# Performance work log

Hardware: AMD Instinct MI355X
Metric: run time of the kernel (lower is better)

The kernel has to match this reference:

```python
import jax, jax.numpy as jnp
import numpy as np

NUM_HEADS = 16
HIDDEN = 1024
HEAD_DIM = HIDDEN // NUM_HEADS


def setup_inputs() -> dict:
    key = jax.random.key(0)
    ks = jax.random.split(key, 8)
    B, S = 4, 1024
    scale = 0.02
    return {
        "hidden_states": jax.random.normal(ks[0], (B, S, HIDDEN), jnp.float32),
        "attention_mask": jnp.zeros((B, 1, 1, S), jnp.float32),
        "Wq": jax.random.normal(ks[1], (HIDDEN, HIDDEN), jnp.float32) * scale,
        "bq": jnp.zeros((HIDDEN,), jnp.float32),
        "Wk": jax.random.normal(ks[2], (HIDDEN, HIDDEN), jnp.float32) * scale,
        "bk": jnp.zeros((HIDDEN,), jnp.float32),
        "Wv": jax.random.normal(ks[3], (HIDDEN, HIDDEN), jnp.float32) * scale,
        "bv": jnp.zeros((HIDDEN,), jnp.float32),
    }


def _split_heads(x):
    # [B,S,H] -> [B,heads,S,head_dim]
    B, S, _ = x.shape
    return x.reshape(B, S, NUM_HEADS, HEAD_DIM).transpose(0, 2, 1, 3)


def reference(hidden_states, attention_mask, Wq, bq, Wk, bk, Wv, bv):
    # torch.nn.Linear convention: y = x @ W.T + b
    q = _split_heads(hidden_states @ Wq.T + bq)
    k = _split_heads(hidden_states @ Wk.T + bk)
    v = _split_heads(hidden_states @ Wv.T + bv)
    scores = jnp.einsum('bhqd,bhkd->bhqk', q, k) * (HEAD_DIM ** -0.5)
    scores = scores + attention_mask  # broadcast [B,1,1,S]
    probs = jax.nn.softmax(scores, axis=-1)
    context = jnp.einsum('bhqk,bhkd->bhqd', probs, v)  # [B,heads,S,head_dim]
    B, _, S, _ = context.shape
    return context.transpose(0, 2, 1, 3).reshape(B, S, HIDDEN)
```

## Files before the change

kernel.cpp:

```cpp
#include <hip/hip_runtime.h>
#include <hip/hip_bf16.h>
#include <stdint.h>

#define NH 16
#define HID 1024
#define HD 64
#define NB 4
#define SS 1024
#define MTOT (NB*SS)

typedef __attribute__((ext_vector_type(8))) short bf16x8;
typedef __attribute__((ext_vector_type(4))) float f32x4;
typedef __attribute__((ext_vector_type(16))) float f32x16;

#define LOG2E 1.44269504088896f

__device__ __forceinline__ unsigned short f2bf(float f) {
  union { float f; unsigned u; } v; v.f = f;
  unsigned u = v.u;
  return (unsigned short)((u + 0x7FFFu + ((u >> 16) & 1u)) >> 16);
}

__device__ __forceinline__ unsigned cvtpk(float lo, float hi) {
  unsigned r;
  asm("v_cvt_pk_bf16_f32 %0, %1, %2" : "=v"(r) : "v"(lo), "v"(hi));
  return r;
}

__device__ __forceinline__ void pl32swap(unsigned &a, unsigned &b) {
  asm("v_permlane32_swap_b32 %0, %1" : "+v"(a), "+v"(b));
}

__device__ __forceinline__ float exp2fast(float x) {
  float r;
  asm("v_exp_f32 %0, %1" : "=v"(r) : "v"(x));
  return r;
}

__device__ __forceinline__ void async16(void* lds, const void* g) {
  __builtin_amdgcn_global_load_lds(
      (const __attribute__((address_space(1))) unsigned*)g,
      (__attribute__((address_space(3))) unsigned*)lds, 16, 0, 0);
}

__global__ void cvt_all(const float4* __restrict__ X,
                        const float4* __restrict__ Wq,
                        const float4* __restrict__ Wk,
                        const float4* __restrict__ Wv,
                        ushort4* __restrict__ Xb,
                        ushort4* __restrict__ Wb) {
  int i = blockIdx.x * 256 + threadIdx.x;
  const float4* src; ushort4* dst; int idx;
  if (i < (MTOT * HID / 4)) {
    src = X; dst = Xb; idx = i;
  } else {
    int j = i - (MTOT * HID / 4);
    int sel = j >> 18;
    idx = j & 262143;
    src = (sel == 0) ? Wq : (sel == 1) ? Wk : Wv;
    dst = Wb + (size_t)sel * 262144;
  }
  float4 v = src[idx];
  ushort4 o;
  o.x = f2bf(v.x); o.y = f2bf(v.y); o.z = f2bf(v.z); o.w = f2bf(v.w);
  dst[idx] = o;
}

__global__ __launch_bounds__(256) void qkv_gemm(
    const ushort* __restrict__ Xb,
    const ushort* __restrict__ Wb,
    const float* __restrict__ bq,
    const float* __restrict__ bk,
    const float* __restrict__ bv,
    ushort* __restrict__ Q,
    ushort* __restrict__ K,
    ushort* __restrict__ Vt)
{
  __shared__ __attribute__((aligned(16))) ushort Al[2][128 * 32];
  __shared__ __attribute__((aligned(16))) ushort Bl[2][128 * 32];

  int bid = blockIdx.x;
  int swz = (bid & 7) * 96 + (bid >> 3);
  const int nbn = 3072 / 128;
  int bm = swz / nbn, bn = swz % nbn;
  int m0 = bm * 128, n0 = bn * 128;

  int tid = threadIdx.x;
  int wave = tid >> 6, lane = tid & 63;
  int g = lane >> 4, c = lane & 15;
  int wr = wave >> 1, wc = wave & 1;

  int srow = tid >> 2;
  int schunk = tid & 3;
  int ssw = (srow >> 1) & 3;
  const ushort* Asrc0 = Xb + (size_t)(m0 + srow) * 1024 + ((schunk ^ ssw) << 3);
  const ushort* Asrc1 = Xb + (size_t)(m0 + 64 + srow) * 1024 + ((schunk ^ ssw) << 3);
  const ushort* Bsrc0 = Wb + (size_t)(n0 + srow) * 1024 + ((schunk ^ ssw) << 3);
  const ushort* Bsrc1 = Wb + (size_t)(n0 + 64 + srow) * 1024 + ((schunk ^ ssw) << 3);
  int soff = srow * 64 + schunk * 16;

#define GSTAGE(bi) do {                                   \
    char* la_ = (char*)Al[bi]; char* lb_ = (char*)Bl[bi]; \
    async16(la_ + soff,        Asrc0);                    \
    async16(la_ + 4096 + soff, Asrc1);                    \
    async16(lb_ + soff,        Bsrc0);                    \
    async16(lb_ + 4096 + soff, Bsrc1);                    \
    Asrc0 += 32; Asrc1 += 32; Bsrc0 += 32; Bsrc1 += 32;   \
  } while (0)

  f32x4 acc[4][4] = {};
  int rsw = (c >> 1) & 3;
  int ch = ((g ^ rsw) << 4);

  GSTAGE(0);

  for (int ks = 0; ks < 32; ++ks) {
    int cur = ks & 1;
    if (ks < 31) {
      GSTAGE(cur ^ 1);
      asm volatile("s_waitcnt vmcnt(4)" ::: "memory");
    } else {
      asm volatile("s_waitcnt vmcnt(0)" ::: "memory");
    }
    __builtin_amdgcn_sched_barrier(0);
    __builtin_amdgcn_s_barrier();
    __builtin_amdgcn_sched_barrier(0);

    const char* la = (const char*)Al[cur];
    const char* lb = (const char*)Bl[cur];
    bf16x8 a[4], b[4];
    #pragma unroll
    for (int m = 0; m < 4; ++m)
      a[m] = *(const bf16x8*)(la + (wr * 64 + m * 16 + c) * 64 + ch);
    #pragma unroll
    for (int n = 0; n < 4; ++n)
      b[n] = *(const bf16x8*)(lb + (wc * 64 + n * 16 + c) * 64 + ch);
    __builtin_amdgcn_s_setprio(1);
    #pragma unroll
    for (int m = 0; m < 4; ++m)
      #pragma unroll
      for (int n = 0; n < 4; ++n)
        acc[m][n] = __builtin_amdgcn_mfma_f32_16x16x32_bf16(a[m], b[n], acc[m][n], 0, 0, 0);
    __builtin_amdgcn_s_setprio(0);

    __builtin_amdgcn_sched_barrier(0);
    __builtin_amdgcn_s_barrier();
  }
#undef GSTAGE

  int sel = n0 >> 10;
  const float* bp = (sel == 0) ? bq : (sel == 1) ? bk : bv;
  float scl = (sel == 0) ? 0.125f * LOG2E : 1.0f;

  #pragma unroll
  for (int n = 0; n < 4; ++n) {
    int nn = (n0 & 1023) + wc * 64 + n * 16 + c;
    float bias = bp[nn];
    int h = nn >> 6, d = nn & 63;
    #pragma unroll
    for (int m = 0; m < 4; ++m) {
      int rowg = m0 + wr * 64 + m * 16 + g * 4;
      int bb = rowg >> 10;
      int s = rowg & 1023;
      #pragma unroll
      for (int r = 0; r < 4; ++r) {
        float val = (acc[m][n][r] + bias) * scl;
        unsigned short ob = f2bf(val);
        if (sel == 0)
          Q[(size_t)((bb * 16 + h) * 1024 + s + r) * 64 + d] = ob;
        else if (sel == 1)
          K[(size_t)((bb * 16 + h) * 1024 + s + r) * 64 + d] = ob;
        else
          Vt[(size_t)((bb * 16 + h) * 64 + d) * 1024 + s + r] = ob;
      }
    }
  }
}

__device__ __forceinline__ void build_pa(const f32x16& p, bf16x8& pa0, bf16x8& pa1) {
  unsigned W0 = cvtpk(p[0],  p[1]);
  unsigned W1 = cvtpk(p[2],  p[3]);
  unsigned W2 = cvtpk(p[4],  p[5]);
  unsigned W3 = cvtpk(p[6],  p[7]);
  unsigned W4 = cvtpk(p[8],  p[9]);
  unsigned W5 = cvtpk(p[10], p[11]);
  unsigned W6 = cvtpk(p[12], p[13]);
  unsigned W7 = cvtpk(p[14], p[15]);
  pl32swap(W0, W2);
  pl32swap(W1, W3);
  pl32swap(W4, W6);
  pl32swap(W5, W7);
  union { unsigned u[4]; bf16x8 v; } a0, a1;
  a0.u[0] = W0; a0.u[1] = W1; a0.u[2] = W2; a0.u[3] = W3;
  a1.u[0] = W4; a1.u[1] = W5; a1.u[2] = W6; a1.u[3] = W7;
  pa0 = a0.v; pa1 = a1.v;
}

__global__ __launch_bounds__(256) void attn(
    const ushort* __restrict__ Q,
    const ushort* __restrict__ K,
    const ushort* __restrict__ Vt,
    const float* __restrict__ mask,
    float* __restrict__ out)
{
  __shared__ __attribute__((aligned(16))) char kv_lds[2][16384];

  int blk = blockIdx.x;
  int xcd = blk & 7;
  int j = blk >> 3;
  int bh = xcd * 8 + (j >> 3);
  int qt = j & 7;
  int b = bh >> 4, h = bh & 15;
  int tid = threadIdx.x, wave = tid >> 6, lane = tid & 63;
  int r31 = lane & 31, hi = lane >> 5;
  int rsw = r31 & 7;
  int hib = hi << 4;
  int q0 = qt * 128 + wave * 32;

  const ushort* Qb = Q + (size_t)bh * SS * 64;
  const ushort* Kb = K + (size_t)bh * SS * 64;
  const ushort* Vb = Vt + (size_t)bh * 64 * SS;
  const float* mb = mask + b * SS;

  bf16x8 qf[4];
  #pragma unroll
  for (int kp = 0; kp < 4; ++kp)
    qf[kp] = *(const bf16x8*)(Qb + (size_t)(q0 + r31) * 64 + kp * 16 + hi * 8);

  int srow = lane >> 3;
  int schunk = lane & 7;
  const ushort* sptr[4];
  int soff[4];
  #pragma unroll
  for (int j2 = 0; j2 < 4; ++j2) {
    soff[j2] = wave * 4096 + j2 * 1024;
    if (wave < 2) {
      int row = wave * 32 + j2 * 8 + srow;
      sptr[j2] = Kb + (size_t)row * 64 + ((schunk ^ srow) << 3);
    } else {
      int d = (wave - 2) * 32 + j2 * 8 + srow;
      sptr[j2] = Vb + (size_t)d * SS + ((schunk ^ srow) << 3);
    }
  }
  const int sstep = (wave < 2) ? 64 * 64 : 64;

#define STAGE(bufidx) do {                              \
    char* lb_ = kv_lds[bufidx];                         \
    async16(lb_ + soff[0], sptr[0]);                    \
    async16(lb_ + soff[1], sptr[1]);                    \
    async16(lb_ + soff[2], sptr[2]);                    \
    async16(lb_ + soff[3], sptr[3]);                    \
    sptr[0] += sstep; sptr[1] += sstep;                 \
    sptr[2] += sstep; sptr[3] += sstep;                 \
  } while (0)

  f32x16 o0 = (f32x16)0.0f, o1 = (f32x16)0.0f;
  float mrow = 0.f, lrow = 0.f;

  STAGE(0);

  for (int it = 0; it < 16; ++it) {
    int cur = it & 1;
    if (it < 15) {
      STAGE(cur ^ 1);
      asm volatile("s_waitcnt vmcnt(4)" ::: "memory");
    } else {
      asm volatile("s_waitcnt vmcnt(0)" ::: "memory");
    }
    __builtin_amdgcn_sched_barrier(0);
    __builtin_amdgcn_s_barrier();
    __builtin_amdgcn_sched_barrier(0);

    const char* kb0 = kv_lds[cur];
    const char* vb0 = kv_lds[cur] + 8192;

    f32x16 s0 = (f32x16)0.0f, s1 = (f32x16)0.0f;
    __builtin_amdgcn_s_setprio(1);
    #pragma unroll
    for (int kp = 0; kp < 4; ++kp) {
      int ch = (((kp << 1) | hi) ^ rsw) << 4;
      bf16x8 ka = *(const bf16x8*)(kb0 + r31 * 128 + ch);
      bf16x8 kc = *(const bf16x8*)(kb0 + (32 + r31) * 128 + ch);
      s0 = __builtin_amdgcn_mfma_f32_32x32x16_bf16(ka, qf[kp], s0, 0, 0, 0);
      s1 = __builtin_amdgcn_mfma_f32_32x32x16_bf16(kc, qf[kp], s1, 0, 0, 0);
    }
    __builtin_amdgcn_s_setprio(0);

    int kv = it * 64;
    #pragma unroll
    for (int sq = 0; sq < 4; ++sq) {
      f32x4 mk0 = *(const f32x4*)(mb + kv + sq * 8 + hi * 4);
      f32x4 mk1 = *(const f32x4*)(mb + kv + 32 + sq * 8 + hi * 4);
      #pragma unroll
      for (int r = 0; r < 4; ++r) {
        s0[sq * 4 + r] = fmaf(mk0[r], LOG2E, s0[sq * 4 + r]);
        s1[sq * 4 + r] = fmaf(mk1[r], LOG2E, s1[sq * 4 + r]);
      }
    }

    float mx = s0[0];
    #pragma unroll
    for (int i = 1; i < 16; ++i) mx = fmaxf(mx, s0[i]);
    #pragma unroll
    for (int i = 0; i < 16; ++i) mx = fmaxf(mx, s1[i]);
    mx = fmaxf(mx, __shfl_xor(mx, 32));

    if (!__all(mx <= mrow + 11.5416f)) {
      float mn = fmaxf(mrow, mx);
      float sc = exp2fast(mrow - mn);
      mrow = mn;
      lrow *= sc;
      #pragma unroll
      for (int i = 0; i < 16; ++i) {
        int qh = (i & 3) + 8 * (i >> 2);
        float scq = __uint_as_float((unsigned)__builtin_amdgcn_ds_bpermute(
            (qh << 2) + hib, (int)__float_as_uint(sc)));
        o0[i] *= scq; o1[i] *= scq;
      }
    }

    f32x16 p0, p1;
    float rs = 0.f;
    #pragma unroll
    for (int i = 0; i < 16; ++i) { float e = exp2fast(s0[i] - mrow); p0[i] = e; rs += e; }
    #pragma unroll
    for (int i = 0; i < 16; ++i) { float e = exp2fast(s1[i] - mrow); p1[i] = e; rs += e; }
    rs += __shfl_xor(rs, 32);
    lrow += rs;

    #pragma unroll
    for (int T = 0; T < 2; ++T) {
      bf16x8 pa0, pa1;
      build_pa(T ? p1 : p0, pa0, pa1);
      __builtin_amdgcn_s_setprio(1);
      #pragma unroll
      for (int kh = 0; kh < 2; ++kh) {
        int kap = 2 * T + kh;
        int ch = (((kap << 1) | hi) ^ rsw) << 4;
        bf16x8 va = *(const bf16x8*)(vb0 + r31 * 128 + ch);
        bf16x8 vc = *(const bf16x8*)(vb0 + (32 + r31) * 128 + ch);
        bf16x8 pf = kh ? pa1 : pa0;
        o0 = __builtin_amdgcn_mfma_f32_32x32x16_bf16(pf, va, o0, 0, 0, 0);
        o1 = __builtin_amdgcn_mfma_f32_32x32x16_bf16(pf, vc, o1, 0, 0, 0);
      }
      __builtin_amdgcn_s_setprio(0);
    }

    __builtin_amdgcn_sched_barrier(0);
    __builtin_amdgcn_s_barrier();
  }
#undef STAGE

  float inv = 1.0f / lrow;
  #pragma unroll
  for (int i = 0; i < 16; ++i) {
    int qh = (i & 3) + 8 * (i >> 2);
    float li = __uint_as_float((unsigned)__builtin_amdgcn_ds_bpermute(
        (qh << 2) + hib, (int)__float_as_uint(inv)));
    int row = q0 + qh + 4 * hi;
    float* op = out + (size_t)(b * SS + row) * 1024 + h * 64 + r31;
    op[0]  = o0[i] * li;
    op[32] = o1[i] * li;
  }
}

extern "C" void kernel_launch(void* const* d_in, const int* in_sizes, int n_in,
                              void* d_out, int out_size, void* d_ws, size_t ws_size,
                              hipStream_t stream) {
  const float* hs   = (const float*)d_in[0];
  const float* mask = (const float*)d_in[1];
  const float* Wq   = (const float*)d_in[2];
  const float* bq   = (const float*)d_in[3];
  const float* Wk   = (const float*)d_in[4];
  const float* bk   = (const float*)d_in[5];
  const float* Wv   = (const float*)d_in[6];
  const float* bv   = (const float*)d_in[7];
  float* out = (float*)d_out;

  char* ws = (char*)d_ws;
  ushort* Xb = (ushort*)(ws);
  ushort* Wb = (ushort*)(ws + (8u  << 20));
  ushort* Qp = (ushort*)(ws + (14u << 20));
  ushort* Kp = (ushort*)(ws + (22u << 20));
  ushort* Vt = (ushort*)(ws + (30u << 20));

  cvt_all<<<7168, 256, 0, stream>>>((const float4*)hs, (const float4*)Wq,
                                    (const float4*)Wk, (const float4*)Wv,
                                    (ushort4*)Xb, (ushort4*)Wb);
  qkv_gemm<<<768, 256, 0, stream>>>(Xb, Wb, bq, bk, bv, Qp, Kp, Vt);
  attn<<<512, 256, 0, stream>>>(Qp, Kp, Vt, mask, out);
}
```

Baseline: 87.15 us.

## Triple-buffer LDS tiles with one barrier per step; stage mask in LDS

Both the QKV GEMM and the attention kernel go from double to triple-buffered LDS tiles. The next stage is issued after the single per-iteration barrier, and the trailing barrier at the end of each loop body is removed. This gives two loads in flight and halves barrier synchronisation per step, at the cost of more LDS per block, which may reduce occupancy. The attention kernel also preloads the mask row, pre-scaled by log2(e), into LDS once per block, replacing per-iteration global mask loads and the fma.

```diff
diff --git a/kernel.cpp b/kernel.cpp
--- a/kernel.cpp
+++ b/kernel.cpp
@@ -76,8 +76,8 @@
     ushort* __restrict__ K,
     ushort* __restrict__ Vt)
 {
-  __shared__ __attribute__((aligned(16))) ushort Al[2][128 * 32];
-  __shared__ __attribute__((aligned(16))) ushort Bl[2][128 * 32];
+  __shared__ __attribute__((aligned(16))) ushort Al[3][128 * 32];
+  __shared__ __attribute__((aligned(16))) ushort Bl[3][128 * 32];
 
   int bid = blockIdx.x;
   int swz = (bid & 7) * 96 + (bid >> 3);
@@ -113,11 +113,11 @@
   int ch = ((g ^ rsw) << 4);
 
   GSTAGE(0);
-
+  GSTAGE(1);
+
+  int cur = 0, nxt = 2;
   for (int ks = 0; ks < 32; ++ks) {
-    int cur = ks & 1;
     if (ks < 31) {
-      GSTAGE(cur ^ 1);
       asm volatile("s_waitcnt vmcnt(4)" ::: "memory");
     } else {
       asm volatile("s_waitcnt vmcnt(0)" ::: "memory");
@@ -125,6 +125,7 @@
     __builtin_amdgcn_sched_barrier(0);
     __builtin_amdgcn_s_barrier();
     __builtin_amdgcn_sched_barrier(0);
+    if (ks < 30) GSTAGE(nxt);
 
     const char* la = (const char*)Al[cur];
     const char* lb = (const char*)Bl[cur];
@@ -143,8 +144,8 @@
         acc[m][n] = __builtin_amdgcn_mfma_f32_16x16x32_bf16(a[m], b[n], acc[m][n], 0, 0, 0);
     __builtin_amdgcn_s_setprio(0);
 
-    __builtin_amdgcn_sched_barrier(0);
-    __builtin_amdgcn_s_barrier();
+    cur = (cur == 2) ? 0 : cur + 1;
+    nxt = (nxt == 2) ? 0 : nxt + 1;
   }
 #undef GSTAGE
 
@@ -203,7 +204,8 @@
     const float* __restrict__ mask,
     float* __restrict__ out)
 {
-  __shared__ __attribute__((aligned(16))) char kv_lds[2][16384];
+  __shared__ __attribute__((aligned(16))) char kv_lds[3][16384];
+  __shared__ float mask_s[SS];
 
   int blk = blockIdx.x;
   int xcd = blk & 7;
@@ -220,7 +222,8 @@
   const ushort* Qb = Q + (size_t)bh * SS * 64;
   const ushort* Kb = K + (size_t)bh * SS * 64;
   const ushort* Vb = Vt + (size_t)bh * 64 * SS;
-  const float* mb = mask + b * SS;
+
+  for (int i = tid; i < SS; i += 256) mask_s[i] = mask[b * SS + i] * LOG2E;
 
   bf16x8 qf[4];
   #pragma unroll
@@ -254,15 +257,16 @@
     sptr[2] += sstep; sptr[3] += sstep;                 \
   } while (0)
 
+  __syncthreads();
+  STAGE(0);
+  STAGE(1);
+
   f32x16 o0 = (f32x16)0.0f, o1 = (f32x16)0.0f;
   float mrow = 0.f, lrow = 0.f;
 
-  STAGE(0);
-
+  int cur = 0, nxt = 2;
   for (int it = 0; it < 16; ++it) {
-    int cur = it & 1;
     if (it < 15) {
-      STAGE(cur ^ 1);
       asm volatile("s_waitcnt vmcnt(4)" ::: "memory");
     } else {
       asm volatile("s_waitcnt vmcnt(0)" ::: "memory");
@@ -270,6 +274,7 @@
     __builtin_amdgcn_sched_barrier(0);
     __builtin_amdgcn_s_barrier();
     __builtin_amdgcn_sched_barrier(0);
+    if (it < 14) STAGE(nxt);
 
     const char* kb0 = kv_lds[cur];
     const char* vb0 = kv_lds[cur] + 8192;
@@ -289,12 +294,12 @@
     int kv = it * 64;
     #pragma unroll
     for (int sq = 0; sq < 4; ++sq) {
-      f32x4 mk0 = *(const f32x4*)(mb + kv + sq * 8 + hi * 4);
-      f32x4 mk1 = *(const f32x4*)(mb + kv + 32 + sq * 8 + hi * 4);
+      f32x4 mk0 = *(const f32x4*)(&mask_s[kv + sq * 8 + hi * 4]);
+      f32x4 mk1 = *(const f32x4*)(&mask_s[kv + 32 + sq * 8 + hi * 4]);
       #pragma unroll
       for (int r = 0; r < 4; ++r) {
-        s0[sq * 4 + r] = fmaf(mk0[r], LOG2E, s0[sq * 4 + r]);
-        s1[sq * 4 + r] = fmaf(mk1[r], LOG2E, s1[sq * 4 + r]);
+        s0[sq * 4 + r] += mk0[r];
+        s1[sq * 4 + r] += mk1[r];
       }
     }
 
@@ -346,8 +351,8 @@
       __builtin_amdgcn_s_setprio(0);
     }
 
-    __builtin_amdgcn_sched_barrier(0);
-    __builtin_amdgcn_s_barrier();
+    cur = (cur == 2) ? 0 : cur + 1;
+    nxt = (nxt == 2) ? 0 : nxt + 1;
   }
 #undef STAGE
 
```

Result: no change. 85.83 us (-1.5%).
